# Optimization experiments

Measured on AMD Instinct MI355X. Metric: run time of the kernel, lower is better.

Reference implementation:

```python
import jax, jax.numpy as jnp
import numpy as np
from jax import lax

N = 100000   # num_nodes
E = 1600000  # num_edges (avg degree 16)
F = 128      # num_features
H = 256      # hidden_channels
C = 64       # num_classes
K = 10       # propagation steps
ALPHA = 0.1
BETA = 0.5
THETA = 0.5
EPS = 1e-5   # BatchNorm eps


def setup_inputs() -> dict:
    key = jax.random.key(0)
    ks = jax.random.split(key, 16)
    x = jax.random.normal(ks[0], (N, F), dtype=jnp.float32)
    src = jax.random.randint(ks[1], (E,), 0, N, dtype=jnp.int32)
    dst = jax.random.randint(ks[2], (E,), 0, N, dtype=jnp.int32)
    # row-normalized adjacency weights so repeated A@z stays bounded
    deg = jax.ops.segment_sum(jnp.ones((E,), jnp.float32), dst, num_segments=N)
    w = (1.0 / jnp.maximum(deg, 1.0))[dst]
    # MLP params (Linear + BatchNorm per hidden layer)
    W1 = jax.random.normal(ks[3], (F, H), dtype=jnp.float32) * 0.05
    b1 = jnp.zeros((H,), jnp.float32)
    g1 = jnp.ones((H,), jnp.float32)
    be1 = jnp.zeros((H,), jnp.float32)
    W2 = jax.random.normal(ks[4], (H, H), dtype=jnp.float32) * 0.05
    b2 = jnp.zeros((H,), jnp.float32)
    g2 = jnp.ones((H,), jnp.float32)
    be2 = jnp.zeros((H,), jnp.float32)
    W3 = jax.random.normal(ks[5], (H, C), dtype=jnp.float32) * 0.05
    b3 = jnp.zeros((C,), jnp.float32)
    # lazy caches (warm-start memories); nonzero so the blend branch is taken
    z_sam = jax.random.normal(ks[6], (N, C), dtype=jnp.float32) * 0.1
    g_sam = jax.random.normal(ks[7], (N, C), dtype=jnp.float32) * 0.01
    return dict(x=x, src=src, dst=dst, w=w,
                W1=W1, b1=b1, g1=g1, be1=be1,
                W2=W2, b2=b2, g2=g2, be2=be2,
                W3=W3, b3=b3, z_sam=z_sam, g_sam=g_sam, size=N)


def _bn(h, gamma, beta):
    # BatchNorm1d in training mode: batch statistics over nodes
    mu = jnp.mean(h, axis=0)
    var = jnp.var(h, axis=0)
    return (h - mu) * jax.lax.rsqrt(var + EPS) * gamma + beta


def reference(x, src, dst, w, W1, b1, g1, be1, W2, b2, g2, be2, W3, b3,
              z_sam, g_sam, size):
    # MLP stack: Linear -> BN -> ReLU (dropout omitted: deterministic reference)
    h = jax.nn.relu(_bn(x @ W1 + b1, g1, be1))
    h = jax.nn.relu(_bn(h @ W2 + b2, g2, be2))
    logits = h @ W3 + b3  # [N, C]

    def spmm(z):
        # (A @ z)_i = sum_{j -> i} w_ij * z_j
        return jax.ops.segment_sum(z[src] * w[:, None], dst, num_segments=N)

    # Lazy_Prop.forward: warm-start blend, then K propagation steps
    use_x = jnp.all(z_sam[:size] == 0.0)
    z0 = jnp.where(use_x, logits, (1.0 - BETA) * z_sam + BETA * logits)
    z = lax.fori_loop(0, K, lambda i, z: (1.0 - ALPHA) * spmm(z) + ALPHA * logits, z0)
    return jax.nn.log_softmax(z, axis=1)
```

## Files before the change

### kernel.cpp

```cpp
#include <hip/hip_runtime.h>
#include <hip/hip_bf16.h>

#define NODES 100000
#define EDGES 1600000
#define FEAT  128
#define HID   256
#define CLS   64
#define KPROP 10
#define ALPHA_C 0.1f
#define BETA_C  0.5f
#define BN_EPS  1e-5f

typedef __attribute__((ext_vector_type(8))) short short8;
typedef __attribute__((ext_vector_type(4))) float f32x4;

static __device__ __forceinline__ unsigned short f2b(float f) {
    __hip_bfloat16 h = __float2bfloat16(f);
    return *(unsigned short*)&h;
}
static __device__ __forceinline__ float b2f(unsigned short u) {
    __hip_bfloat16 h;
    *(unsigned short*)&h = u;
    return __bfloat162float(h);
}
static __device__ __forceinline__ float asf(unsigned int u) {
    union { unsigned int u; float f; } c; c.u = u; return c.f;
}

__global__ void packwt_k(const float* __restrict__ W, unsigned short* __restrict__ Wt,
                         int K, int N)
{
    int i = blockIdx.x * 256 + threadIdx.x;
    if (i < K * N) {
        int k = i / N, n = i - k * N;
        Wt[(size_t)n * K + k] = f2b(W[i]);
    }
}

template<bool AF32, bool FUSE, bool STATS, bool OUTF32, int KK, bool COLSPLIT>
__global__ __launch_bounds__(256, 2)
void gemm_stream_k(const void* __restrict__ Ain, const unsigned short* __restrict__ Wt,
                   const float* __restrict__ bias,
                   const float* __restrict__ scale, const float* __restrict__ shift,
                   void* __restrict__ outp,
                   float* __restrict__ gsum, float* __restrict__ gsq,
                   int M, int N)
{
    const int lane = threadIdx.x & 63;
    const int wv   = threadIdx.x >> 6;
    const int quad = lane >> 4;
    const int l16  = lane & 15;
    constexpr int NK8 = KK / 32;

    int rbase, colbase;
    if constexpr (COLSPLIT) { rbase = blockIdx.x * 32;             colbase = wv * 64; }
    else                    { rbase = (blockIdx.x * 4 + wv) * 32;  colbase = 0;       }

    short8 Bf[4][NK8];
    #pragma unroll
    for (int ct = 0; ct < 4; ++ct) {
        const unsigned short* wp = Wt + (size_t)(colbase + ct * 16 + l16) * KK + quad * 8;
        #pragma unroll
        for (int ks = 0; ks < NK8; ++ks)
            Bf[ct][ks] = *(const short8*)(wp + ks * 32);
    }

    f32x4 acc[2][4];
    #pragma unroll
    for (int i = 0; i < 2; ++i)
        #pragma unroll
        for (int j = 0; j < 4; ++j)
            acc[i][j] = (f32x4){0.f, 0.f, 0.f, 0.f};

    #pragma unroll
    for (int ks = 0; ks < NK8; ++ks) {
        const int k = ks * 32 + quad * 8;
        float sc[8], sh[8];
        if constexpr (FUSE) {
            float4 s0 = *(const float4*)(scale + k);
            float4 s1 = *(const float4*)(scale + k + 4);
            float4 h0 = *(const float4*)(shift + k);
            float4 h1 = *(const float4*)(shift + k + 4);
            sc[0]=s0.x; sc[1]=s0.y; sc[2]=s0.z; sc[3]=s0.w;
            sc[4]=s1.x; sc[5]=s1.y; sc[6]=s1.z; sc[7]=s1.w;
            sh[0]=h0.x; sh[1]=h0.y; sh[2]=h0.z; sh[3]=h0.w;
            sh[4]=h1.x; sh[5]=h1.y; sh[6]=h1.z; sh[7]=h1.w;
        }
        short8 a[2];
        #pragma unroll
        for (int rt = 0; rt < 2; ++rt) {
            int row = rbase + rt * 16 + l16;
            float v[8];
            if (row < M) {
                if constexpr (AF32) {
                    const float* ap = (const float*)Ain + (size_t)row * KK + k;
                    float4 t0 = *(const float4*)ap;
                    float4 t1 = *(const float4*)(ap + 4);
                    v[0]=t0.x; v[1]=t0.y; v[2]=t0.z; v[3]=t0.w;
                    v[4]=t1.x; v[5]=t1.y; v[6]=t1.z; v[7]=t1.w;
                } else {
                    short8 t = *(const short8*)((const unsigned short*)Ain + (size_t)row * KK + k);
                    #pragma unroll
                    for (int j = 0; j < 8; ++j) v[j] = b2f((unsigned short)t[j]);
                }
            } else {
                #pragma unroll
                for (int j = 0; j < 8; ++j) v[j] = 0.f;
            }
            if constexpr (FUSE) {
                #pragma unroll
                for (int j = 0; j < 8; ++j) v[j] = fmaxf(fmaf(v[j], sc[j], sh[j]), 0.f);
            }
            short8 av;
            #pragma unroll
            for (int j = 0; j < 8; ++j) av[j] = (short)f2b(v[j]);
            a[rt] = av;
        }
        #pragma unroll
        for (int ct = 0; ct < 4; ++ct) {
            acc[0][ct] = __builtin_amdgcn_mfma_f32_16x16x32_bf16(a[0], Bf[ct][ks], acc[0][ct], 0, 0, 0);
            acc[1][ct] = __builtin_amdgcn_mfma_f32_16x16x32_bf16(a[1], Bf[ct][ks], acc[1][ct], 0, 0, 0);
        }
    }

    float ps[4] = {0.f, 0.f, 0.f, 0.f};
    float pq[4] = {0.f, 0.f, 0.f, 0.f};
    #pragma unroll
    for (int ct = 0; ct < 4; ++ct) {
        int col = colbase + ct * 16 + l16;
        float bcol = bias[col];
        #pragma unroll
        for (int rt = 0; rt < 2; ++rt) {
            #pragma unroll
            for (int r2 = 0; r2 < 4; ++r2) {
                int row = rbase + rt * 16 + quad * 4 + r2;
                float v = acc[rt][ct][r2] + bcol;
                if (row < M) {
                    if constexpr (STATS) { ps[ct] += v; pq[ct] += v * v; }
                    if constexpr (OUTF32) {
                        ((float*)outp)[(size_t)row * N + col] = v;
                    } else {
                        ((unsigned short*)outp)[(size_t)row * N + col] = f2b(v);
                    }
                }
            }
        }
    }
    if constexpr (STATS) {
        #pragma unroll
        for (int ct = 0; ct < 4; ++ct) {
            float s = ps[ct];
            s += __shfl_xor(s, 16, 64);
            s += __shfl_xor(s, 32, 64);
            float q = pq[ct];
            q += __shfl_xor(q, 16, 64);
            q += __shfl_xor(q, 32, 64);
            if (lane < 16) {
                atomicAdd(&gsum[colbase + ct * 16 + lane], s);
                atomicAdd(&gsq[colbase + ct * 16 + lane], q);
            }
        }
    }
}

__global__ void bnfin_k(const float* __restrict__ sum, const float* __restrict__ sq,
                        const float* __restrict__ g, const float* __restrict__ be,
                        float* __restrict__ scale, float* __restrict__ shift)
{
    int c = threadIdx.x;
    float mu = sum[c] * (1.f / NODES);
    float var = sq[c] * (1.f / NODES) - mu * mu;
    float sc = g[c] * rsqrtf(var + BN_EPS);
    scale[c] = sc;
    shift[c] = be[c] - mu * sc;
}

__global__ void flag_k(const float* __restrict__ zs, int* __restrict__ flag)
{
    int i = blockIdx.x * 256 + threadIdx.x;
    bool nz = (i < NODES * CLS) && (zs[i] != 0.f);
    if (__any(nz)) {
        if ((threadIdx.x & 63) == 0) *flag = 1;
    }
}

__global__ void blend_k(const float* __restrict__ zs, const float* __restrict__ logits,
                        const int* __restrict__ flag, unsigned short* __restrict__ z0)
{
    int i = blockIdx.x * 256 + threadIdx.x;
    if (i < NODES * CLS) {
        float l = logits[i];
        float v = (*flag) ? ((1.f - BETA_C) * zs[i] + BETA_C * l) : l;
        z0[i] = f2b(v);
    }
}

__global__ void count_k(const int* __restrict__ dst, int* __restrict__ cnt)
{
    int i = blockIdx.x * 256 + threadIdx.x;
    if (i < EDGES) atomicAdd(&cnt[dst[i]], 1);
}

__global__ void scan1_k(const int* __restrict__ cnt, int* __restrict__ rowptr,
                        int* __restrict__ bsum)
{
    __shared__ int s[256];
    int tid = threadIdx.x;
    int i = blockIdx.x * 256 + tid;
    int v = (i < NODES) ? cnt[i] : 0;
    s[tid] = v;
    __syncthreads();
    for (int off = 1; off < 256; off <<= 1) {
        int t = (tid >= off) ? s[tid - off] : 0;
        __syncthreads();
        s[tid] += t;
        __syncthreads();
    }
    if (i < NODES) rowptr[i] = s[tid] - v;
    if (tid == 255) bsum[blockIdx.x] = s[255];
}

__global__ void scan2_k(const int* __restrict__ bsum, int* __restrict__ boffs, int nb)
{
    __shared__ int s[512];
    int tid = threadIdx.x;
    int v = (tid < nb) ? bsum[tid] : 0;
    s[tid] = v;
    __syncthreads();
    for (int off = 1; off < 512; off <<= 1) {
        int t = (tid >= off) ? s[tid - off] : 0;
        __syncthreads();
        s[tid] += t;
        __syncthreads();
    }
    if (tid < nb) boffs[tid] = s[tid] - v;
}

__global__ void scan3_k(int* __restrict__ rowptr, const int* __restrict__ boffs,
                        int* __restrict__ cursor)
{
    int i = blockIdx.x * 256 + threadIdx.x;
    if (i < NODES) {
        int v = rowptr[i] + boffs[blockIdx.x];
        rowptr[i] = v;
        cursor[i] = v;
    }
    if (i == 0) rowptr[NODES] = EDGES;
}

__global__ void fill_k(const int* __restrict__ src, const int* __restrict__ dst,
                       int* __restrict__ cursor, int* __restrict__ esrc)
{
    int i = blockIdx.x * 256 + threadIdx.x;
    if (i < EDGES) {
        int pos = atomicAdd(&cursor[dst[i]], 1);
        esrc[pos] = src[i];
    }
}

__global__ __launch_bounds__(256)
void prop_k(const int* __restrict__ rowptr, const int* __restrict__ esrc,
            const unsigned int* __restrict__ zin, const float* __restrict__ logits,
            unsigned int* __restrict__ zout)
{
    int row = blockIdx.x * 8 + (threadIdx.x >> 5);
    if (row >= NODES) return;
    int l32 = threadIdx.x & 31;
    int beg = rowptr[row], end = rowptr[row + 1];
    float acc0 = 0.f, acc1 = 0.f;

    for (int cbeg = beg; cbeg < end; cbeg += 32) {
        int e = cbeg + l32;
        int s_l = (e < end) ? esrc[e] : 0;
        int cnt = min(32, end - cbeg);
        int j = 0;
        for (; j + 8 <= cnt; j += 8) {
            int idx[8];
            #pragma unroll
            for (int u = 0; u < 8; ++u) idx[u] = __shfl(s_l, j + u, 32);
            unsigned int vv[8];
            #pragma unroll
            for (int u = 0; u < 8; ++u)
                vv[u] = __hip_atomic_load(zin + (size_t)idx[u] * 32 + l32,
                                          __ATOMIC_RELAXED, __HIP_MEMORY_SCOPE_AGENT);
            #pragma unroll
            for (int u = 0; u < 8; ++u) {
                acc0 += asf(vv[u] << 16);
                acc1 += asf(vv[u] & 0xffff0000u);
            }
        }
        for (; j < cnt; ++j) {
            int s0 = __shfl(s_l, j, 32);
            unsigned int v = __hip_atomic_load(zin + (size_t)s0 * 32 + l32,
                                               __ATOMIC_RELAXED, __HIP_MEMORY_SCOPE_AGENT);
            acc0 += asf(v << 16);
            acc1 += asf(v & 0xffff0000u);
        }
    }
    float dg = (float)(end - beg);
    float inv = 1.f / fmaxf(dg, 1.f);
    float2 lv = *(const float2*)(logits + (size_t)row * CLS + l32 * 2);
    float r0 = (1.f - ALPHA_C) * inv * acc0 + ALPHA_C * lv.x;
    float r1 = (1.f - ALPHA_C) * inv * acc1 + ALPHA_C * lv.y;
    zout[(size_t)row * 32 + l32] = ((unsigned int)f2b(r1) << 16) | (unsigned int)f2b(r0);
}

__global__ __launch_bounds__(256)
void logsoftmax_k(const unsigned short* __restrict__ z, float* __restrict__ out)
{
    int row = blockIdx.x * 4 + (threadIdx.x >> 6);
    if (row >= NODES) return;
    int lane = threadIdx.x & 63;
    float v = b2f(z[(size_t)row * CLS + lane]);
    float m = v;
    #pragma unroll
    for (int off = 32; off > 0; off >>= 1) m = fmaxf(m, __shfl_xor(m, off, 64));
    float ex = expf(v - m);
    float s = ex;
    #pragma unroll
    for (int off = 32; off > 0; off >>= 1) s += __shfl_xor(s, off, 64);
    out[(size_t)row * CLS + lane] = (v - m) - logf(s);
}

extern "C" void kernel_launch(void* const* d_in, const int* in_sizes, int n_in,
                              void* d_out, int out_size, void* d_ws, size_t ws_size,
                              hipStream_t stream)
{
    const float* x   = (const float*)d_in[0];
    const int*   src = (const int*)d_in[1];
    const int*   dst = (const int*)d_in[2];
    const float* W1  = (const float*)d_in[4];
    const float* b1  = (const float*)d_in[5];
    const float* g1  = (const float*)d_in[6];
    const float* be1 = (const float*)d_in[7];
    const float* W2  = (const float*)d_in[8];
    const float* b2  = (const float*)d_in[9];
    const float* g2  = (const float*)d_in[10];
    const float* be2 = (const float*)d_in[11];
    const float* W3  = (const float*)d_in[12];
    const float* b3  = (const float*)d_in[13];
    const float* zsam = (const float*)d_in[14];
    float* outp = (float*)d_out;

    uint8_t* base = (uint8_t*)d_ws;
    float* s_scale1 = (float*)(base);
    float* s_shift1 = s_scale1 + 256;
    float* s_scale2 = s_shift1 + 256;
    float* s_shift2 = s_scale2 + 256;
    float* s_sum    = s_shift2 + 256;
    float* s_sq     = s_sum + 256;
    int*   flag     = (int*)(s_sq + 256);

    unsigned short* Wt1 = (unsigned short*)(base + (1 << 14));
    unsigned short* Wt2 = Wt1 + (size_t)FEAT * HID;
    unsigned short* Wt3 = Wt2 + (size_t)HID * HID;
    unsigned short* h1  = Wt3 + (size_t)HID * CLS;
    unsigned short* h2  = h1 + (size_t)NODES * HID;
    float* logits = (float*)(h2 + (size_t)NODES * HID);
    unsigned short* zA  = (unsigned short*)(logits + (size_t)NODES * CLS);
    unsigned short* zB  = zA + (size_t)NODES * CLS;
    int* esrc   = (int*)(zB + (size_t)NODES * CLS);
    int* rowptr = esrc + EDGES;
    int* cursor = rowptr + (NODES + 1);
    int* cnt    = cursor + NODES;
    int* bsum   = cnt + NODES;
    int* boffs  = bsum + 512;

    const int STRIPS = (NODES + 31) / 32;
    const int SCANB  = (NODES + 255) / 256;

    packwt_k<<<(FEAT * HID + 255) / 256, 256, 0, stream>>>(W1, Wt1, FEAT, HID);
    packwt_k<<<(HID * HID + 255) / 256, 256, 0, stream>>>(W2, Wt2, HID, HID);
    packwt_k<<<(HID * CLS + 255) / 256, 256, 0, stream>>>(W3, Wt3, HID, CLS);

    hipMemsetAsync(cnt, 0, NODES * sizeof(int), stream);
    count_k<<<(EDGES + 255) / 256, 256, 0, stream>>>(dst, cnt);
    scan1_k<<<SCANB, 256, 0, stream>>>(cnt, rowptr, bsum);
    scan2_k<<<1, 512, 0, stream>>>(bsum, boffs, SCANB);
    scan3_k<<<SCANB, 256, 0, stream>>>(rowptr, boffs, cursor);
    fill_k<<<(EDGES + 255) / 256, 256, 0, stream>>>(src, dst, cursor, esrc);

    hipMemsetAsync(s_sum, 0, 512 * sizeof(float), stream);
    gemm_stream_k<true, false, true, false, FEAT, true><<<STRIPS, 256, 0, stream>>>(
        x, Wt1, b1, nullptr, nullptr, h1, s_sum, s_sq, NODES, HID);
    bnfin_k<<<1, 256, 0, stream>>>(s_sum, s_sq, g1, be1, s_scale1, s_shift1);

    hipMemsetAsync(s_sum, 0, 512 * sizeof(float), stream);
    gemm_stream_k<false, true, true, false, HID, true><<<STRIPS, 256, 0, stream>>>(
        h1, Wt2, b2, s_scale1, s_shift1, h2, s_sum, s_sq, NODES, HID);
    bnfin_k<<<1, 256, 0, stream>>>(s_sum, s_sq, g2, be2, s_scale2, s_shift2);

    gemm_stream_k<false, true, false, true, HID, false><<<(STRIPS + 3) / 4, 256, 0, stream>>>(
        h2, Wt3, b3, s_scale2, s_shift2, logits, nullptr, nullptr, NODES, CLS);

    hipMemsetAsync(flag, 0, sizeof(int), stream);
    flag_k<<<(NODES * CLS + 255) / 256, 256, 0, stream>>>(zsam, flag);
    blend_k<<<(NODES * CLS + 255) / 256, 256, 0, stream>>>(zsam, logits, flag, zA);

    const int PROPB = (NODES + 7) / 8;
    for (int it = 0; it < KPROP; ++it) {
        const unsigned int* zi = (const unsigned int*)((it & 1) ? zB : zA);
        unsigned int* zo = (unsigned int*)((it & 1) ? zA : zB);
        prop_k<<<PROPB, 256, 0, stream>>>(rowptr, esrc, zi, logits, zo);
    }

    logsoftmax_k<<<(NODES + 3) / 4, 256, 0, stream>>>(zA, outp);
}
```

Baseline: 1.020 ms.

## Stage GEMM weights in swizzled LDS and loop blocks over row chunks

Replaces the register-resident weight GEMM with a kernel that loads a 64-column weight slice once per block into XOR-swizzled shared memory. Each block then loops over several 128-row chunks, so weight loading and bias/stat setup are amortized and the per-block stat atomics are reduced. All A-fragment loads for a tile are issued up front, and BN scale/shift are cached in LDS. In exchange the kernel adds LDS reads in the inner loop and runs with fewer blocks. For the 128-row input tiles on the first two layers, blocks are spread across 4 column groups, so each A tile is read by four blocks.

```diff
diff --git a/kernel.cpp b/kernel.cpp
--- a/kernel.cpp
+++ b/kernel.cpp
@@ -37,115 +37,162 @@
     }
 }
 
-template<bool AF32, bool FUSE, bool STATS, bool OUTF32, int KK, bool COLSPLIT>
-__global__ __launch_bounds__(256, 2)
-void gemm_stream_k(const void* __restrict__ Ain, const unsigned short* __restrict__ Wt,
-                   const float* __restrict__ bias,
-                   const float* __restrict__ scale, const float* __restrict__ shift,
-                   void* __restrict__ outp,
-                   float* __restrict__ gsum, float* __restrict__ gsq,
-                   int M, int N)
-{
+template<bool AF32, bool FUSE, bool STATS, bool OUTF32, int KK, int NCOLG>
+__global__ __launch_bounds__(256, 3)
+void gemm_lds_k(const void* __restrict__ Ain, const unsigned short* __restrict__ Wt,
+                const float* __restrict__ bias,
+                const float* __restrict__ scale, const float* __restrict__ shift,
+                void* __restrict__ outp,
+                float* __restrict__ gsum, float* __restrict__ gsq,
+                int M, int N, int nchunks, int nblk)
+{
+    constexpr int NK8 = KK / 32;
+    __shared__ unsigned short Blds[64 * KK];
+    __shared__ float Slds[KK];
+    __shared__ float Hlds[KK];
+
     const int lane = threadIdx.x & 63;
     const int wv   = threadIdx.x >> 6;
     const int quad = lane >> 4;
     const int l16  = lane & 15;
-    constexpr int NK8 = KK / 32;
-
-    int rbase, colbase;
-    if constexpr (COLSPLIT) { rbase = blockIdx.x * 32;             colbase = wv * 64; }
-    else                    { rbase = (blockIdx.x * 4 + wv) * 32;  colbase = 0;       }
-
-    short8 Bf[4][NK8];
+    const int colg = (NCOLG > 1) ? (blockIdx.x % NCOLG) : 0;
+    const int blk0 = (NCOLG > 1) ? (blockIdx.x / NCOLG) : blockIdx.x;
+    const int colbase = colg * 64;
+
+    {
+        const unsigned short* wp = Wt + (size_t)colbase * KK;
+        constexpr int ELEMS = 64 * KK / 8;
+        #pragma unroll
+        for (int i0 = 0; i0 < ELEMS; i0 += 256) {
+            int i  = i0 + threadIdx.x;
+            int c  = i / (KK / 8);
+            int k8 = i - c * (KK / 8);
+            short8 v = *(const short8*)(wp + (size_t)c * KK + k8 * 8);
+            int byte = c * (KK * 2) + ((k8 * 16) ^ ((c & 7) << 4));
+            *(short8*)((char*)Blds + byte) = v;
+        }
+        if constexpr (FUSE) {
+            for (int i = threadIdx.x; i < KK; i += 256) {
+                Slds[i] = scale[i];
+                Hlds[i] = shift[i];
+            }
+        }
+    }
+    __syncthreads();
+
+    float bcol[4];
     #pragma unroll
-    for (int ct = 0; ct < 4; ++ct) {
-        const unsigned short* wp = Wt + (size_t)(colbase + ct * 16 + l16) * KK + quad * 8;
-        #pragma unroll
-        for (int ks = 0; ks < NK8; ++ks)
-            Bf[ct][ks] = *(const short8*)(wp + ks * 32);
-    }
-
-    f32x4 acc[2][4];
-    #pragma unroll
-    for (int i = 0; i < 2; ++i)
-        #pragma unroll
-        for (int j = 0; j < 4; ++j)
-            acc[i][j] = (f32x4){0.f, 0.f, 0.f, 0.f};
-
-    #pragma unroll
-    for (int ks = 0; ks < NK8; ++ks) {
-        const int k = ks * 32 + quad * 8;
-        float sc[8], sh[8];
-        if constexpr (FUSE) {
-            float4 s0 = *(const float4*)(scale + k);
-            float4 s1 = *(const float4*)(scale + k + 4);
-            float4 h0 = *(const float4*)(shift + k);
-            float4 h1 = *(const float4*)(shift + k + 4);
-            sc[0]=s0.x; sc[1]=s0.y; sc[2]=s0.z; sc[3]=s0.w;
-            sc[4]=s1.x; sc[5]=s1.y; sc[6]=s1.z; sc[7]=s1.w;
-            sh[0]=h0.x; sh[1]=h0.y; sh[2]=h0.z; sh[3]=h0.w;
-            sh[4]=h1.x; sh[5]=h1.y; sh[6]=h1.z; sh[7]=h1.w;
-        }
-        short8 a[2];
+    for (int ct = 0; ct < 4; ++ct) bcol[ct] = bias[colbase + ct * 16 + l16];
+
+    float ps[4] = {0.f, 0.f, 0.f, 0.f};
+    float pq[4] = {0.f, 0.f, 0.f, 0.f};
+
+    for (int chunk = blk0; chunk < nchunks; chunk += nblk) {
+        const int rbase = chunk * 128 + wv * 32;
+
+        f32x4 acc[2][4];
+        #pragma unroll
+        for (int i = 0; i < 2; ++i)
+            #pragma unroll
+            for (int j = 0; j < 4; ++j)
+                acc[i][j] = (f32x4){0.f, 0.f, 0.f, 0.f};
+
+        short8 abf[2][NK8];
+        float4 af[2][NK8][2];
         #pragma unroll
         for (int rt = 0; rt < 2; ++rt) {
-            int row = rbase + rt * 16 + l16;
-            float v[8];
-            if (row < M) {
+            const int row = rbase + rt * 16 + l16;
+            const bool ok = row < M;
+            if constexpr (AF32) {
+                const float* ap = (const float*)Ain + (size_t)row * KK + quad * 8;
+                #pragma unroll
+                for (int ks = 0; ks < NK8; ++ks) {
+                    if (ok) {
+                        af[rt][ks][0] = *(const float4*)(ap + ks * 32);
+                        af[rt][ks][1] = *(const float4*)(ap + ks * 32 + 4);
+                    } else {
+                        af[rt][ks][0] = (float4){0.f, 0.f, 0.f, 0.f};
+                        af[rt][ks][1] = (float4){0.f, 0.f, 0.f, 0.f};
+                    }
+                }
+            } else {
+                const unsigned short* ap = (const unsigned short*)Ain + (size_t)row * KK + quad * 8;
+                #pragma unroll
+                for (int ks = 0; ks < NK8; ++ks) {
+                    if (ok) abf[rt][ks] = *(const short8*)(ap + ks * 32);
+                    else    abf[rt][ks] = (short8){0, 0, 0, 0, 0, 0, 0, 0};
+                }
+            }
+        }
+
+        #pragma unroll
+        for (int ks = 0; ks < NK8; ++ks) {
+            const int k = ks * 32 + quad * 8;
+            float sc[8], sh[8];
+            if constexpr (FUSE) {
+                float4 s0 = *(const float4*)&Slds[k];
+                float4 s1 = *(const float4*)&Slds[k + 4];
+                float4 h0 = *(const float4*)&Hlds[k];
+                float4 h1 = *(const float4*)&Hlds[k + 4];
+                sc[0]=s0.x; sc[1]=s0.y; sc[2]=s0.z; sc[3]=s0.w;
+                sc[4]=s1.x; sc[5]=s1.y; sc[6]=s1.z; sc[7]=s1.w;
+                sh[0]=h0.x; sh[1]=h0.y; sh[2]=h0.z; sh[3]=h0.w;
+                sh[4]=h1.x; sh[5]=h1.y; sh[6]=h1.z; sh[7]=h1.w;
+            }
+            short8 a2[2];
+            #pragma unroll
+            for (int rt = 0; rt < 2; ++rt) {
+                float v[8];
                 if constexpr (AF32) {
-                    const float* ap = (const float*)Ain + (size_t)row * KK + k;
-                    float4 t0 = *(const float4*)ap;
-                    float4 t1 = *(const float4*)(ap + 4);
+                    float4 t0 = af[rt][ks][0];
+                    float4 t1 = af[rt][ks][1];
                     v[0]=t0.x; v[1]=t0.y; v[2]=t0.z; v[3]=t0.w;
                     v[4]=t1.x; v[5]=t1.y; v[6]=t1.z; v[7]=t1.w;
                 } else {
-                    short8 t = *(const short8*)((const unsigned short*)Ain + (size_t)row * KK + k);
                     #pragma unroll
-                    for (int j = 0; j < 8; ++j) v[j] = b2f((unsigned short)t[j]);
+                    for (int j = 0; j < 8; ++j) v[j] = b2f((unsigned short)abf[rt][ks][j]);
                 }
-            } else {
+                if constexpr (FUSE) {
+                    #pragma unroll
+                    for (int j = 0; j < 8; ++j) v[j] = fmaxf(fmaf(v[j], sc[j], sh[j]), 0.f);
+                }
+                short8 av;
                 #pragma unroll
-                for (int j = 0; j < 8; ++j) v[j] = 0.f;
-            }
-            if constexpr (FUSE) {
+                for (int j = 0; j < 8; ++j) av[j] = (short)f2b(v[j]);
+                a2[rt] = av;
+            }
+            #pragma unroll
+            for (int ct = 0; ct < 4; ++ct) {
+                const int boff = (ct * 16 + l16) * (KK * 2)
+                               + ((ks * 64 + quad * 16) ^ ((l16 & 7) << 4));
+                short8 bf = *(const short8*)((const char*)Blds + boff);
+                acc[0][ct] = __builtin_amdgcn_mfma_f32_16x16x32_bf16(a2[0], bf, acc[0][ct], 0, 0, 0);
+                acc[1][ct] = __builtin_amdgcn_mfma_f32_16x16x32_bf16(a2[1], bf, acc[1][ct], 0, 0, 0);
+            }
+        }
+
+        #pragma unroll
+        for (int ct = 0; ct < 4; ++ct) {
+            const int col = colbase + ct * 16 + l16;
+            #pragma unroll
+            for (int rt = 0; rt < 2; ++rt) {
                 #pragma unroll
-                for (int j = 0; j < 8; ++j) v[j] = fmaxf(fmaf(v[j], sc[j], sh[j]), 0.f);
-            }
-            short8 av;
-            #pragma unroll
-            for (int j = 0; j < 8; ++j) av[j] = (short)f2b(v[j]);
-            a[rt] = av;
-        }
-        #pragma unroll
-        for (int ct = 0; ct < 4; ++ct) {
-            acc[0][ct] = __builtin_amdgcn_mfma_f32_16x16x32_bf16(a[0], Bf[ct][ks], acc[0][ct], 0, 0, 0);
-            acc[1][ct] = __builtin_amdgcn_mfma_f32_16x16x32_bf16(a[1], Bf[ct][ks], acc[1][ct], 0, 0, 0);
-        }
-    }
-
-    float ps[4] = {0.f, 0.f, 0.f, 0.f};
-    float pq[4] = {0.f, 0.f, 0.f, 0.f};
-    #pragma unroll
-    for (int ct = 0; ct < 4; ++ct) {
-        int col = colbase + ct * 16 + l16;
-        float bcol = bias[col];
-        #pragma unroll
-        for (int rt = 0; rt < 2; ++rt) {
-            #pragma unroll
-            for (int r2 = 0; r2 < 4; ++r2) {
-                int row = rbase + rt * 16 + quad * 4 + r2;
-                float v = acc[rt][ct][r2] + bcol;
-                if (row < M) {
-                    if constexpr (STATS) { ps[ct] += v; pq[ct] += v * v; }
-                    if constexpr (OUTF32) {
-                        ((float*)outp)[(size_t)row * N + col] = v;
-                    } else {
-                        ((unsigned short*)outp)[(size_t)row * N + col] = f2b(v);
+                for (int r2 = 0; r2 < 4; ++r2) {
+                    const int row = rbase + rt * 16 + quad * 4 + r2;
+                    if (row < M) {
+                        float v = acc[rt][ct][r2] + bcol[ct];
+                        if constexpr (STATS) { ps[ct] += v; pq[ct] += v * v; }
+                        if constexpr (OUTF32) {
+                            ((float*)outp)[(size_t)row * N + col] = v;
+                        } else {
+                            ((unsigned short*)outp)[(size_t)row * N + col] = f2b(v);
+                        }
                     }
                 }
             }
         }
     }
+
     if constexpr (STATS) {
         #pragma unroll
         for (int ct = 0; ct < 4; ++ct) {
@@ -366,7 +413,8 @@
     int* bsum   = cnt + NODES;
     int* boffs  = bsum + 512;
 
-    const int STRIPS = (NODES + 31) / 32;
+    const int NCHUNK = (NODES + 127) / 128;
+    const int NBLK   = (NCHUNK + 1) / 2;
     const int SCANB  = (NODES + 255) / 256;
 
     packwt_k<<<(FEAT * HID + 255) / 256, 256, 0, stream>>>(W1, Wt1, FEAT, HID);
@@ -381,17 +429,17 @@
     fill_k<<<(EDGES + 255) / 256, 256, 0, stream>>>(src, dst, cursor, esrc);
 
     hipMemsetAsync(s_sum, 0, 512 * sizeof(float), stream);
-    gemm_stream_k<true, false, true, false, FEAT, true><<<STRIPS, 256, 0, stream>>>(
-        x, Wt1, b1, nullptr, nullptr, h1, s_sum, s_sq, NODES, HID);
+    gemm_lds_k<true, false, true, false, FEAT, 4><<<NBLK * 4, 256, 0, stream>>>(
+        x, Wt1, b1, nullptr, nullptr, h1, s_sum, s_sq, NODES, HID, NCHUNK, NBLK);
     bnfin_k<<<1, 256, 0, stream>>>(s_sum, s_sq, g1, be1, s_scale1, s_shift1);
 
     hipMemsetAsync(s_sum, 0, 512 * sizeof(float), stream);
-    gemm_stream_k<false, true, true, false, HID, true><<<STRIPS, 256, 0, stream>>>(
-        h1, Wt2, b2, s_scale1, s_shift1, h2, s_sum, s_sq, NODES, HID);
+    gemm_lds_k<false, true, true, false, HID, 4><<<NBLK * 4, 256, 0, stream>>>(
+        h1, Wt2, b2, s_scale1, s_shift1, h2, s_sum, s_sq, NODES, HID, NCHUNK, NBLK);
     bnfin_k<<<1, 256, 0, stream>>>(s_sum, s_sq, g2, be2, s_scale2, s_shift2);
 
-    gemm_stream_k<false, true, false, true, HID, false><<<(STRIPS + 3) / 4, 256, 0, stream>>>(
-        h2, Wt3, b3, s_scale2, s_shift2, logits, nullptr, nullptr, NODES, CLS);
+    gemm_lds_k<false, true, false, true, HID, 1><<<NCHUNK, 256, 0, stream>>>(
+        h2, Wt3, b3, s_scale2, s_shift2, logits, nullptr, nullptr, NODES, CLS, NCHUNK, NCHUNK);
 
     hipMemsetAsync(flag, 0, sizeof(int), stream);
     flag_k<<<(NODES * CLS + 255) / 256, 256, 0, stream>>>(zsam, flag);
```

New measurement: 1.210 ms. 18.6% more time.
